# Kernel tuning notes

Measured on AMD Instinct MI355X. Metric: run time of the kernel, lower is better.

The kernel has to match this reference:

```python
import jax, jax.numpy as jnp
import numpy as np

# ---- DMP constants (from DMPParameters with N=5, tau=1, dt=1/(T*l), Dof=9, a_z=25) ----
N_BASIS = 5
T_STEPS = 10
L_SUB = 10
DIM = 9                      # len(state_index)
TAU = 1.0
DT = TAU / (T_STEPS * L_SUB)            # 0.01
TIME_STEPS = int(round(TAU / DT)) + 1   # 101
A_X = 1.0
A_Z = 25.0
B_Z = A_Z / 4.0
_c_np = np.exp(-A_X * np.linspace(0.0, 1.0, N_BASIS))
C = jnp.asarray(_c_np, dtype=jnp.float32)                          # rbf centers
H = jnp.asarray(N_BASIS ** 1.5 / _c_np / A_X, dtype=jnp.float32)   # rbf widths (sigma2)


def _integrate(w, y0, dy0, goal):
    """Euler integration of the DMP dynamical system.
    w: (R, N) basis weights; y0, dy0, goal: (R,) with R = batch*DIM.
    Returns Y: (R, TIME_STEPS) positions."""
    scale = goal - y0  # fixed forcing-term scaling

    def step(carry, _):
        y, z, x = carry
        x = x + (-A_X * x / TAU) * DT                  # canonical system
        psi = jnp.exp(-H * (x - C) ** 2)               # (N,) gaussian rbf
        fx = (w @ psi) * x * scale / jnp.sum(psi)      # (R,) forcing term
        dz = (A_Z * (B_Z * (goal - y) - z) + fx) / TAU
        dy = z / TAU
        y = y + dy * DT
        z = z + dz * DT
        return (y, z, x), y

    z0 = dy0 * TAU
    _, ys = jax.lax.scan(step, (y0, z0, jnp.float32(1.0)), None, length=TIME_STEPS - 1)
    # prepend initial position, transpose to (R, TIME_STEPS)
    return jnp.concatenate([y0[None, :], ys], axis=0).T


def setup_inputs():
    key = jax.random.key(0)
    ks = jax.random.split(key, 4)
    B, D_IN, HID = 16384, 128, 2048
    out_size = DIM * (N_BASIS + 1)  # 54 = N*dim + dim
    return {
        "input": jax.random.normal(ks[0], (B, D_IN), jnp.float32),
        "W0": jax.random.normal(ks[1], (HID, D_IN), jnp.float32) / np.sqrt(D_IN),
        "b0": jnp.full((HID,), 0.1, jnp.float32),
        "W1": jax.random.normal(ks[2], (HID, HID), jnp.float32) / np.sqrt(HID),
        "b1": jnp.full((HID,), 0.1, jnp.float32),
        "Wl": jax.random.normal(ks[3], (out_size, HID), jnp.float32) / np.sqrt(HID),
        "bl": jnp.zeros((out_size,), jnp.float32),
    }


def reference(input, W0, b0, W1, b1, Wl, bl):
    B = input.shape[0]
    # MLP backbone with tanh hidden activation
    h = jnp.tanh(input @ W0.T + b0)
    h = jnp.tanh(h @ W1.T + b1)
    out = (h @ Wl.T + bl) * 100.0                          # (B, DIM*(N+1))
    # split DMP parameters: goal then basis weights
    goal = out[:, :DIM].reshape(-1)                        # (B*DIM,)
    w = out[:, DIM:DIM * (N_BASIS + 1)].reshape(-1, N_BASIS)  # (B*DIM, N)
    y0 = input[:, 7:16].reshape(-1)                        # state_index
    dy0 = input[:, 22:31].reshape(-1)                      # vel_index
    Y = _integrate(w, y0, dy0, goal)                       # (B*DIM, 101)
    y = Y.reshape(B, DIM, TIME_STEPS)[:, :, ::L_SUB]       # (B, DIM, T+1)
    return y[:, :, 1:] - y[:, :, :-1]                      # (B, DIM, T)
```

## Files before the change

kernel.cpp:

```cpp
#include <hip/hip_runtime.h>
#include <hip/hip_fp16.h>
#include <math.h>

typedef _Float16 f16;
typedef _Float16 f16x8 __attribute__((ext_vector_type(8)));
typedef _Float16 f16x4v __attribute__((ext_vector_type(4)));
typedef float f32x4 __attribute__((ext_vector_type(4)));

#define B_SZ 16384
#define D_INP 128
#define HID 2048
#define DIMS 9
#define OUTC 54
#define OUTP 64
#define NZ3 4

__device__ __forceinline__ void load_lds16(const f16* g, f16* l) {
    __builtin_amdgcn_global_load_lds(
        (__attribute__((address_space(1))) void*)(g),
        (__attribute__((address_space(3))) void*)(l),
        16, 0, 0);
}

__device__ __forceinline__ float fast_tanh(float x) {
    float e = __builtin_amdgcn_exp2f(2.885390081777927f * x);
    return 1.0f - 2.0f * __builtin_amdgcn_rcpf(e + 1.0f);
}

template <int BN, int EPI>
__global__ __launch_bounds__(256, 2) void gemm_nt(
    const f16* __restrict__ A, const f16* __restrict__ Bm,
    const float* __restrict__ bias, void* __restrict__ Cout,
    int M, int N, int K, int bias_n)
{
    constexpr int BM = 128, BK = 64;
    constexpr int NI = BN / 32;
    __shared__ __align__(16) f16 sa[BM * BK];
    __shared__ __align__(16) f16 sb[BN * BK];

    const int tid  = threadIdx.x;
    const int lane = tid & 63;
    const int wave = tid >> 6;
    const int wm = wave >> 1, wn = wave & 1;

    const int flat = blockIdx.x + blockIdx.y * gridDim.x;
    const int gsz  = 8 * gridDim.y;
    const int grp  = flat / gsz;
    const int rem  = flat - grp * gsz;
    const int m0 = (grp * 8 + (rem & 7)) * BM;
    const int n0 = (rem >> 3) * BN;

    const int k_len = K / gridDim.z;
    const int k_beg = blockIdx.z * k_len;
    const int k_end = k_beg + k_len;

    f32x4 acc[4][NI];
    #pragma unroll
    for (int i = 0; i < 4; ++i)
        #pragma unroll
        for (int j = 0; j < NI; ++j) acc[i][j] = (f32x4){0.f, 0.f, 0.f, 0.f};

    const int r8 = lane >> 3;
    const int cg = (((lane & 7) ^ r8) << 3);

    for (int k0 = k_beg; k0 < k_end; k0 += BK) {
        #pragma unroll
        for (int c = 0; c < (BM * BK * 2) / 4096; ++c) {
            int o = c * 4096 + wave * 1024;
            const f16* gp = A + (size_t)(m0 + (o >> 7) + r8) * K + k0 + cg;
            load_lds16(gp, (f16*)((char*)sa + o));
        }
        #pragma unroll
        for (int c = 0; c < (BN * BK * 2) / 4096; ++c) {
            int o = c * 4096 + wave * 1024;
            const f16* gp = Bm + (size_t)(n0 + (o >> 7) + r8) * K + k0 + cg;
            load_lds16(gp, (f16*)((char*)sb + o));
        }
        __syncthreads();

        #pragma unroll
        for (int kc = 0; kc < 2; ++kc) {
            f16x8 af[4], bf[NI];
            #pragma unroll
            for (int mi = 0; mi < 4; ++mi) {
                int ar = wm * 64 + mi * 16 + (lane & 15);
                af[mi] = *(const f16x8*)&sa[ar * 64 + ((((kc << 2) | (lane >> 4)) ^ (ar & 7)) << 3)];
            }
            #pragma unroll
            for (int ni = 0; ni < NI; ++ni) {
                int br = wn * (BN / 2) + ni * 16 + (lane & 15);
                bf[ni] = *(const f16x8*)&sb[br * 64 + ((((kc << 2) | (lane >> 4)) ^ (br & 7)) << 3)];
            }
            #pragma unroll
            for (int mi = 0; mi < 4; ++mi)
                #pragma unroll
                for (int ni = 0; ni < NI; ++ni)
                    acc[mi][ni] = __builtin_amdgcn_mfma_f32_16x16x32_f16(af[mi], bf[ni], acc[mi][ni], 0, 0, 0);
        }
        __syncthreads();
    }

    const int crow0 = m0 + wm * 64 + (lane >> 4) * 4;
    const int ccol0 = n0 + wn * (BN / 2) + (lane & 15);
    if (EPI == 0) {
        f16* C = (f16*)Cout;
        #pragma unroll
        for (int mi = 0; mi < 4; ++mi)
            #pragma unroll
            for (int ni = 0; ni < NI; ++ni) {
                int col = ccol0 + ni * 16;
                float bv = bias[col];
                #pragma unroll
                for (int r2 = 0; r2 < 4; ++r2) {
                    float v = fast_tanh(acc[mi][ni][r2] + bv);
                    C[(size_t)(crow0 + mi * 16 + r2) * N + col] = (f16)v;
                }
            }
    } else {
        float* C = (float*)Cout + (size_t)blockIdx.z * M * N;
        #pragma unroll
        for (int mi = 0; mi < 4; ++mi)
            #pragma unroll
            for (int ni = 0; ni < NI; ++ni) {
                int col = ccol0 + ni * 16;
                float bv = (blockIdx.z == 0 && col < bias_n) ? bias[col] * 100.0f : 0.0f;
                #pragma unroll
                for (int r2 = 0; r2 < 4; ++r2) {
                    float v = acc[mi][ni][r2] * 100.0f + bv;
                    C[(size_t)(crow0 + mi * 16 + r2) * N + col] = v;
                }
            }
    }
}

__global__ __launch_bounds__(256, 2) void gemm1_fused(
    const float* __restrict__ A, const float* __restrict__ W0,
    const float* __restrict__ bias,
    const float* __restrict__ W1, const float* __restrict__ Wl,
    f16* __restrict__ w1q, f16* __restrict__ wlq,
    f16* __restrict__ C)
{
    constexpr int NI = 4;
    constexpr int N = HID, K = D_INP;
    __shared__ __align__(16) f16 sa[128 * 128];
    __shared__ __align__(16) f16 sb[128 * 128];

    const int tid  = threadIdx.x;
    const int lane = tid & 63;
    const int wave = tid >> 6;
    const int wm = wave >> 1, wn = wave & 1;
    const int m0 = blockIdx.x * 128;
    const int n0 = blockIdx.y * 128;
    const int bid = blockIdx.x + blockIdx.y * gridDim.x;

    {
        int i0 = bid * 512 + tid;
        #pragma unroll
        for (int j = 0; j < 2; ++j) {
            int idx = i0 + j * 256;
            float4 v = ((const float4*)W1)[idx];
            f16x4v o; o.x = (f16)v.x; o.y = (f16)v.y; o.z = (f16)v.z; o.w = (f16)v.w;
            ((f16x4v*)w1q)[idx] = o;
        }
        if (bid < 128) {
            int idx = bid * 256 + tid;
            int row = (idx * 4) >> 11;
            f16x4v o;
            if (row < OUTC) {
                float4 v = ((const float4*)Wl)[idx];
                o.x = (f16)v.x; o.y = (f16)v.y; o.z = (f16)v.z; o.w = (f16)v.w;
            } else {
                o.x = (f16)0.f; o.y = (f16)0.f; o.z = (f16)0.f; o.w = (f16)0.f;
            }
            ((f16x4v*)wlq)[idx] = o;
        }
    }

    f32x4 acc[4][NI];
    #pragma unroll
    for (int i = 0; i < 4; ++i)
        #pragma unroll
        for (int j = 0; j < NI; ++j) acc[i][j] = (f32x4){0.f, 0.f, 0.f, 0.f};

    #pragma unroll
    for (int c = 0; c < 8; ++c) {
        int o = c * 4096 + wave * 1024;
        int row = (o >> 8) + (lane >> 4);
        int gch = (lane & 15) ^ (row & 15);
        {
            const float* gp = A + (size_t)(m0 + row) * K + gch * 8;
            float4 v0 = *(const float4*)gp;
            float4 v1 = *(const float4*)(gp + 4);
            f16x8 h;
            h[0] = (f16)v0.x; h[1] = (f16)v0.y; h[2] = (f16)v0.z; h[3] = (f16)v0.w;
            h[4] = (f16)v1.x; h[5] = (f16)v1.y; h[6] = (f16)v1.z; h[7] = (f16)v1.w;
            *(f16x8*)((char*)sa + o + (lane << 4)) = h;
        }
        {
            const float* gp = W0 + (size_t)(n0 + row) * K + gch * 8;
            float4 v0 = *(const float4*)gp;
            float4 v1 = *(const float4*)(gp + 4);
            f16x8 h;
            h[0] = (f16)v0.x; h[1] = (f16)v0.y; h[2] = (f16)v0.z; h[3] = (f16)v0.w;
            h[4] = (f16)v1.x; h[5] = (f16)v1.y; h[6] = (f16)v1.z; h[7] = (f16)v1.w;
            *(f16x8*)((char*)sb + o + (lane << 4)) = h;
        }
    }
    __syncthreads();

    #pragma unroll
    for (int kc = 0; kc < 4; ++kc) {
        const int ch = (kc << 2) | (lane >> 4);
        f16x8 af[4], bf[NI];
        #pragma unroll
        for (int mi = 0; mi < 4; ++mi) {
            int ar = wm * 64 + mi * 16 + (lane & 15);
            af[mi] = *(const f16x8*)&sa[ar * 128 + ((ch ^ (ar & 15)) << 3)];
        }
        #pragma unroll
        for (int ni = 0; ni < NI; ++ni) {
            int br = wn * 64 + ni * 16 + (lane & 15);
            bf[ni] = *(const f16x8*)&sb[br * 128 + ((ch ^ (br & 15)) << 3)];
        }
        #pragma unroll
        for (int mi = 0; mi < 4; ++mi)
            #pragma unroll
            for (int ni = 0; ni < NI; ++ni)
                acc[mi][ni] = __builtin_amdgcn_mfma_f32_16x16x32_f16(af[mi], bf[ni], acc[mi][ni], 0, 0, 0);
    }

    const int crow0 = m0 + wm * 64 + (lane >> 4) * 4;
    const int ccol0 = n0 + wn * 64 + (lane & 15);
    #pragma unroll
    for (int mi = 0; mi < 4; ++mi)
        #pragma unroll
        for (int ni = 0; ni < NI; ++ni) {
            int col = ccol0 + ni * 16;
            float bv = bias[col];
            #pragma unroll
            for (int r2 = 0; r2 < 4; ++r2) {
                float v = fast_tanh(acc[mi][ni][r2] + bv);
                C[(size_t)(crow0 + mi * 16 + r2) * N + col] = (f16)v;
            }
        }
}

__global__ __launch_bounds__(256) void integrate_kernel(
    const float* __restrict__ out3p, const float* __restrict__ input,
    float* __restrict__ out)
{
    __shared__ float g[500];
    {
        int k = threadIdx.x;
        if (k < 100) {
            float x = expf(-0.010050335853501441f * (float)(k + 1));
            float psi[5], ssum = 0.0f;
            #pragma unroll
            for (int n = 0; n < 5; ++n) {
                float c = expf(-0.25f * (float)n);
                float h = 11.180339887498949f / c;
                float dx = x - c;
                psi[n] = expf(-h * dx * dx);
                ssum += psi[n];
            }
            float inv = x / ssum;
            #pragma unroll
            for (int n = 0; n < 5; ++n) g[k * 5 + n] = psi[n] * inv;
        }
    }
    __syncthreads();

    int r = blockIdx.x * 256 + threadIdx.x;
    int b = r / DIMS, d = r - b * DIMS;

    float goal = 0.f, w0 = 0.f, w1 = 0.f, w2 = 0.f, w3 = 0.f, w4 = 0.f;
    #pragma unroll
    for (int z = 0; z < NZ3; ++z) {
        const float* ob = out3p + (size_t)z * B_SZ * OUTP + (size_t)b * OUTP;
        goal += ob[d];
        w0 += ob[DIMS + d * 5 + 0];
        w1 += ob[DIMS + d * 5 + 1];
        w2 += ob[DIMS + d * 5 + 2];
        w3 += ob[DIMS + d * 5 + 3];
        w4 += ob[DIMS + d * 5 + 4];
    }

    float y = input[(size_t)b * D_INP + 7 + d];
    float z = input[(size_t)b * D_INP + 22 + d];
    const float scale = goal - y;

    float prev = y;
    float* op = out + (size_t)b * (DIMS * 10) + d * 10;
    int j = 0;
    for (int k = 0; k < 100; ++k) {
        const float* gk = &g[k * 5];
        float fx = scale * (w0 * gk[0] + w1 * gk[1] + w2 * gk[2] + w3 * gk[3] + w4 * gk[4]);
        float dz = 25.0f * (6.25f * (goal - y) - z) + fx;
        y = y + z * 0.01f;
        z = z + dz * 0.01f;
        if ((k % 10) == 9) { op[j] = y - prev; prev = y; ++j; }
    }
}

extern "C" void kernel_launch(void* const* d_in, const int* in_sizes, int n_in,
                              void* d_out, int out_size, void* d_ws, size_t ws_size,
                              hipStream_t stream) {
    (void)in_sizes; (void)n_in; (void)out_size; (void)ws_size;
    const float* input = (const float*)d_in[0];
    const float* W0 = (const float*)d_in[1];
    const float* b0 = (const float*)d_in[2];
    const float* W1 = (const float*)d_in[3];
    const float* b1 = (const float*)d_in[4];
    const float* Wl = (const float*)d_in[5];
    const float* bl = (const float*)d_in[6];
    float* out = (float*)d_out;

    f16* w1q = (f16*)d_ws;
    f16* wlq = w1q + (size_t)HID * HID;
    f16* h1  = wlq + (size_t)OUTP * HID;
    f16* h2  = h1 + (size_t)B_SZ * HID;
    float* out3p = (float*)h1;

    gemm1_fused<<<dim3(B_SZ / 128, HID / 128), 256, 0, stream>>>(
        input, W0, b0, W1, Wl, w1q, wlq, h1);
    gemm_nt<128, 0><<<dim3(B_SZ / 128, HID / 128, 1), 256, 0, stream>>>(
        h1, w1q, b1, (void*)h2, B_SZ, HID, HID, HID);
    gemm_nt<64, 1><<<dim3(B_SZ / 128, 1, NZ3), 256, 0, stream>>>(
        h2, wlq, bl, (void*)out3p, B_SZ, OUTP, HID, OUTC);

    integrate_kernel<<<B_SZ * DIMS / 256, 256, 0, stream>>>(out3p, input, out);
}
```

Baseline: 286.2 us.

## Split gemm1 K loop into BK=64 chunks, group-swizzle blocks, raise split-K for final GEMM

The first fused GEMM now loads its 128-wide K dimension in two 64-wide chunks with a matching XOR swizzle, which halves its LDS footprint from 64KB to 32KB per block so more blocks can be resident. Blocks are remapped in groups of 8 along M for better L2 locality on A and W0. The split-K factor NZ3 for the output GEMM doubles from 4 to 8 to expose more parallelism, at the cost of extra partial-sum traffic and an extra barrier per K chunk.

```diff
diff --git a/kernel.cpp b/kernel.cpp
--- a/kernel.cpp
+++ b/kernel.cpp
@@ -13,7 +13,7 @@
 #define DIMS 9
 #define OUTC 54
 #define OUTP 64
-#define NZ3 4
+#define NZ3 8
 
 __device__ __forceinline__ void load_lds16(const f16* g, f16* l) {
     __builtin_amdgcn_global_load_lds(
@@ -140,17 +140,16 @@
     f16* __restrict__ w1q, f16* __restrict__ wlq,
     f16* __restrict__ C)
 {
-    constexpr int NI = 4;
+    constexpr int BM = 128, BK = 64, BN = 128, NI = 4;
     constexpr int N = HID, K = D_INP;
-    __shared__ __align__(16) f16 sa[128 * 128];
-    __shared__ __align__(16) f16 sb[128 * 128];
+    __shared__ __align__(16) f16 sa[BM * BK];
+    __shared__ __align__(16) f16 sb[BN * BK];
 
     const int tid  = threadIdx.x;
     const int lane = tid & 63;
     const int wave = tid >> 6;
     const int wm = wave >> 1, wn = wave & 1;
-    const int m0 = blockIdx.x * 128;
-    const int n0 = blockIdx.y * 128;
+
     const int bid = blockIdx.x + blockIdx.y * gridDim.x;
 
     {
@@ -176,19 +175,27 @@
         }
     }
 
+    const int flat = bid;
+    const int gsz  = 8 * gridDim.y;
+    const int grp  = flat / gsz;
+    const int rem  = flat - grp * gsz;
+    const int m0 = (grp * 8 + (rem & 7)) * BM;
+    const int n0 = (rem >> 3) * BN;
+
     f32x4 acc[4][NI];
     #pragma unroll
     for (int i = 0; i < 4; ++i)
         #pragma unroll
         for (int j = 0; j < NI; ++j) acc[i][j] = (f32x4){0.f, 0.f, 0.f, 0.f};
 
-    #pragma unroll
-    for (int c = 0; c < 8; ++c) {
-        int o = c * 4096 + wave * 1024;
-        int row = (o >> 8) + (lane >> 4);
-        int gch = (lane & 15) ^ (row & 15);
-        {
-            const float* gp = A + (size_t)(m0 + row) * K + gch * 8;
+    const int r8 = lane >> 3;
+    const int cg = (((lane & 7) ^ r8) << 3);
+
+    for (int k0 = 0; k0 < K; k0 += BK) {
+        #pragma unroll
+        for (int c = 0; c < (BM * BK * 2) / 4096; ++c) {
+            int o = c * 4096 + wave * 1024;
+            const float* gp = A + (size_t)(m0 + (o >> 7) + r8) * K + k0 + cg;
             float4 v0 = *(const float4*)gp;
             float4 v1 = *(const float4*)(gp + 4);
             f16x8 h;
@@ -196,8 +203,10 @@
             h[4] = (f16)v1.x; h[5] = (f16)v1.y; h[6] = (f16)v1.z; h[7] = (f16)v1.w;
             *(f16x8*)((char*)sa + o + (lane << 4)) = h;
         }
-        {
-            const float* gp = W0 + (size_t)(n0 + row) * K + gch * 8;
+        #pragma unroll
+        for (int c = 0; c < (BN * BK * 2) / 4096; ++c) {
+            int o = c * 4096 + wave * 1024;
+            const float* gp = W0 + (size_t)(n0 + (o >> 7) + r8) * K + k0 + cg;
             float4 v0 = *(const float4*)gp;
             float4 v1 = *(const float4*)(gp + 4);
             f16x8 h;
@@ -205,28 +214,28 @@
             h[4] = (f16)v1.x; h[5] = (f16)v1.y; h[6] = (f16)v1.z; h[7] = (f16)v1.w;
             *(f16x8*)((char*)sb + o + (lane << 4)) = h;
         }
-    }
-    __syncthreads();
-
-    #pragma unroll
-    for (int kc = 0; kc < 4; ++kc) {
-        const int ch = (kc << 2) | (lane >> 4);
-        f16x8 af[4], bf[NI];
-        #pragma unroll
-        for (int mi = 0; mi < 4; ++mi) {
-            int ar = wm * 64 + mi * 16 + (lane & 15);
-            af[mi] = *(const f16x8*)&sa[ar * 128 + ((ch ^ (ar & 15)) << 3)];
-        }
-        #pragma unroll
-        for (int ni = 0; ni < NI; ++ni) {
-            int br = wn * 64 + ni * 16 + (lane & 15);
-            bf[ni] = *(const f16x8*)&sb[br * 128 + ((ch ^ (br & 15)) << 3)];
-        }
-        #pragma unroll
-        for (int mi = 0; mi < 4; ++mi)
-            #pragma unroll
-            for (int ni = 0; ni < NI; ++ni)
-                acc[mi][ni] = __builtin_amdgcn_mfma_f32_16x16x32_f16(af[mi], bf[ni], acc[mi][ni], 0, 0, 0);
+        __syncthreads();
+
+        #pragma unroll
+        for (int kc = 0; kc < 2; ++kc) {
+            f16x8 af[4], bf[NI];
+            #pragma unroll
+            for (int mi = 0; mi < 4; ++mi) {
+                int ar = wm * 64 + mi * 16 + (lane & 15);
+                af[mi] = *(const f16x8*)&sa[ar * 64 + ((((kc << 2) | (lane >> 4)) ^ (ar & 7)) << 3)];
+            }
+            #pragma unroll
+            for (int ni = 0; ni < NI; ++ni) {
+                int br = wn * 64 + ni * 16 + (lane & 15);
+                bf[ni] = *(const f16x8*)&sb[br * 64 + ((((kc << 2) | (lane >> 4)) ^ (br & 7)) << 3)];
+            }
+            #pragma unroll
+            for (int mi = 0; mi < 4; ++mi)
+                #pragma unroll
+                for (int ni = 0; ni < NI; ++ni)
+                    acc[mi][ni] = __builtin_amdgcn_mfma_f32_16x16x32_f16(af[mi], bf[ni], acc[mi][ni], 0, 0, 0);
+        }
+        __syncthreads();
     }
 
     const int crow0 = m0 + wm * 64 + (lane >> 4) * 4;
```

Measured after the change: 265.7 us. -7.2%, faster.
